# Optimization experiments

Measured on AMD Instinct MI355X. Metric: run time of the kernel, lower is better.

The kernel has to match this reference:

```python
import math
import jax, jax.numpy as jnp
import numpy as np

D = 1152      # vision_dim
P = 14        # patch
IMG = 896     # image_size
CIN = 3       # vision_channels
L = 2         # vision_blocks
MLP = 4304    # vision_mlp_hidden
EPS = 1e-6
B = 1
N = (IMG // P) ** 2  # 4096 tokens


def _ln(x, w, b):
    m = jnp.mean(x, axis=-1, keepdims=True)
    v = jnp.mean(jnp.square(x - m), axis=-1, keepdims=True)
    return (x - m) * jax.lax.rsqrt(v + EPS) * w + b


def setup_inputs() -> dict:
    key = jax.random.key(0)
    ks = jax.random.split(key, 20)
    s = 0.02
    inp = {
        "img": jax.random.normal(ks[0], (B, CIN, IMG, IMG), jnp.float32),
        "patch_w": jax.random.normal(ks[1], (D, CIN, P, P), jnp.float32) * s,
        "patch_b": jnp.zeros((D,), jnp.float32),
        "pos": jax.random.normal(ks[2], (D, N), jnp.float32) * s,
        # per-block params stacked along leading L axis (torch Linear: [out, in])
        "ln1_w": jnp.ones((L, D), jnp.float32),
        "ln1_b": jnp.zeros((L, D), jnp.float32),
        "qkv_w": jax.random.normal(ks[3], (L, 3 * D, D), jnp.float32) * s,
        "qkv_b": jnp.zeros((L, 3 * D), jnp.float32),
        "proj_w": jax.random.normal(ks[4], (L, D, D), jnp.float32) * s,
        "proj_b": jnp.zeros((L, D), jnp.float32),
        "ln2_w": jnp.ones((L, D), jnp.float32),
        "ln2_b": jnp.zeros((L, D), jnp.float32),
        "fc1_w": jax.random.normal(ks[5], (L, MLP, D), jnp.float32) * s,
        "fc1_b": jnp.zeros((L, MLP), jnp.float32),
        "fc2_w": jax.random.normal(ks[6], (L, D, MLP), jnp.float32) * s,
        "fc2_b": jnp.zeros((L, D), jnp.float32),
        "post_w": jnp.ones((D,), jnp.float32),
        "post_b": jnp.zeros((D,), jnp.float32),
    }
    return inp


def reference(img, patch_w, patch_b, pos, ln1_w, ln1_b, qkv_w, qkv_b,
              proj_w, proj_b, ln2_w, ln2_b, fc1_w, fc1_b, fc2_w, fc2_b,
              post_w, post_b):
    # conv patch embed (kernel=stride=P, valid padding)
    x = jax.lax.conv_general_dilated(
        img, patch_w, window_strides=(P, P), padding="VALID",
        dimension_numbers=("NCHW", "OIHW", "NCHW"))
    x = x + patch_b[None, :, None, None]
    x = x.reshape(B, D, N).transpose(0, 2, 1)          # [B, N, D]
    x = x + pos.T[None, :, :]

    scale = 1.0 / math.sqrt(D)

    def blk(x, p):
        l1w, l1b, qw, qb, pw, pb, l2w, l2b, f1w, f1b, f2w, f2b = p
        h = _ln(x, l1w, l1b)
        qkv = jnp.einsum("bnd,ed->bne", h, qw) + qb     # [B, N, 3D]
        q, k, v = jnp.split(qkv, 3, axis=-1)            # single-head, full D
        attn = jax.nn.softmax(jnp.einsum("bnd,bmd->bnm", q, k) * scale, axis=-1)
        y = jnp.einsum("bnm,bmd->bnd", attn, v)
        x = x + jnp.einsum("bnd,ed->bne", y, pw) + pb
        h = _ln(x, l2w, l2b)
        h = jax.nn.gelu(jnp.einsum("bnd,md->bnm", h, f1w) + f1b, approximate=False)
        x = x + jnp.einsum("bnm,dm->bnd", h, f2w) + f2b
        return x, None

    x, _ = jax.lax.scan(blk, x, (ln1_w, ln1_b, qkv_w, qkv_b, proj_w, proj_b,
                                 ln2_w, ln2_b, fc1_w, fc1_b, fc2_w, fc2_b))
    return _ln(x, post_w, post_b)
```

## Files before the change

### kernel.cpp

```cpp
#include <hip/hip_runtime.h>

#define NT 4096
#define DD 1152
#define D3 3456
#define MLP_R 4304
#define MLP_P 4352
#define KP 640

typedef unsigned short u16;
typedef short v8s __attribute__((ext_vector_type(8)));
typedef float v4f __attribute__((ext_vector_type(4)));

__device__ __forceinline__ u16 f2b(float f) {
    unsigned int u = __builtin_bit_cast(unsigned int, f);
    u += 0x7fffu + ((u >> 16) & 1u);
    return (u16)(u >> 16);
}
__device__ __forceinline__ float b2f(u16 s) {
    unsigned int u = ((unsigned int)s) << 16;
    return __builtin_bit_cast(float, u);
}

__device__ __forceinline__ void async16(const void* g, void* l) {
    __builtin_amdgcn_global_load_lds(
        (const __attribute__((address_space(1))) void*)g,
        (__attribute__((address_space(3))) void*)l, 16, 0, 0);
}

template<int EPI, int MT, int DBUF = 0>
__global__ __launch_bounds__(256)
void gemm_bt(const u16* __restrict__ A, int lda,
             const u16* __restrict__ B, int ldb, int Kdim,
             const float* __restrict__ bias, const float* __restrict__ aux,
             float* __restrict__ outf, u16* __restrict__ outb, int ldc,
             u16* __restrict__ vt, int NX)
{
    constexpr int JT = (MT == 128) ? 4 : 2;
    constexpr int AR = MT * 8 / 256;
    constexpr int NB = DBUF ? 2 : 1;

    __shared__ union SM {
        struct { u16 a[NB * MT * 64]; u16 b[NB * 128 * 64]; } st;
        float sc[4][64][17];
    } sm;

    const int b    = blockIdx.x;
    const int MY   = (gridDim.x >> 3) / NX;
    const int q    = b >> 3;
    const int m0   = ((b & 7) * MY + q % MY) * MT;
    const int n0   = (q / MY) * 128;

    const int tid  = threadIdx.x;
    const int lane = tid & 63;
    const int wave = tid >> 6;
    const int wm   = (MT == 128) ? (wave & 1) * 64 : 0;
    const int wn   = (MT == 128) ? (wave >> 1) * 64 : wave * 32;
    const int fr   = lane & 15;
    const int kqh  = lane >> 4;
    const int swz  = fr & 7;

    v4f acc[4][JT];
    const v4f vzero = {0.f, 0.f, 0.f, 0.f};
#pragma unroll
    for (int i = 0; i < 4; ++i)
#pragma unroll
        for (int j = 0; j < JT; ++j) acc[i][j] = vzero;

    auto stage = [&](u16* As, u16* Bs, int kt) {
#pragma unroll
        for (int r = 0; r < AR; ++r) {
            int c = r * 256 + tid;
            int row = c >> 3;
            int kc = (c & 7) ^ (row & 7);
            async16(A + (size_t)(m0 + row) * lda + kt + kc * 8, As + c * 8);
        }
#pragma unroll
        for (int r = 0; r < 4; ++r) {
            int c = r * 256 + tid;
            int row = c >> 3;
            int kc = (c & 7) ^ (row & 7);
            async16(B + (size_t)(n0 + row) * ldb + kt + kc * 8, Bs + c * 8);
        }
    };

    auto compute = [&](const u16* As, const u16* Bs) {
#pragma unroll
        for (int ks = 0; ks < 2; ++ks) {
            const int kq = ks * 4 + kqh;
            const int kp = (kq ^ swz) * 8;
            v8s af[4], bf[JT];
#pragma unroll
            for (int i = 0; i < 4; ++i)
                af[i] = *(const v8s*)(As + (wm + i * 16 + fr) * 64 + kp);
#pragma unroll
            for (int j = 0; j < JT; ++j)
                bf[j] = *(const v8s*)(Bs + (wn + j * 16 + fr) * 64 + kp);
#pragma unroll
            for (int i = 0; i < 4; ++i)
#pragma unroll
                for (int j = 0; j < JT; ++j)
                    acc[i][j] = __builtin_amdgcn_mfma_f32_16x16x32_bf16(
                        af[i], bf[j], acc[i][j], 0, 0, 0);
        }
    };

    if constexpr (DBUF) {
        stage(sm.st.a, sm.st.b, 0);
        int cur = 0;
        for (int kt = 0; kt < Kdim; kt += 64) {
            __syncthreads();
            const int nxt = cur ^ 1;
            if (kt + 64 < Kdim)
                stage(sm.st.a + nxt * (MT * 64), sm.st.b + nxt * (128 * 64), kt + 64);
            compute(sm.st.a + cur * (MT * 64), sm.st.b + cur * (128 * 64));
            cur = nxt;
        }
    } else {
        for (int kt = 0; kt < Kdim; kt += 64) {
            stage(sm.st.a, sm.st.b, kt);
            __syncthreads();
            compute(sm.st.a, sm.st.b);
            __syncthreads();
        }
    }

    const int cn = lane & 15;
    const int cm = (lane >> 4) * 4;
    float (*S)[17] = sm.sc[wave];
    const int gm = m0 + wm + lane;
#pragma unroll
    for (int jp = 0; jp < JT; ++jp) {
        __syncthreads();
#pragma unroll
        for (int i = 0; i < 4; ++i)
#pragma unroll
            for (int r = 0; r < 4; ++r)
                S[i * 16 + cm + r][cn] = acc[i][jp][r];
        __syncthreads();
        const int gn0 = n0 + wn + jp * 16;
        float v[16];
#pragma unroll
        for (int c = 0; c < 16; ++c) v[c] = S[lane][c];
        if constexpr (EPI <= 2) {
            union { u16 us[16]; uint4 q4[2]; } o;
#pragma unroll
            for (int c = 0; c < 16; ++c) {
                float t = v[c];
                if constexpr (EPI >= 1) t += bias[gn0 + c];
                if constexpr (EPI == 2) {
                    float u = t * (0.7978845608028654f + 0.03567740814183026f * t * t);
                    t = t / (1.0f + __expf(-2.0f * u));
                }
                o.us[c] = f2b(t);
            }
            uint4* dst = (uint4*)(outb + (size_t)gm * ldc + gn0);
            dst[0] = o.q4[0];
            dst[1] = o.q4[1];
            if constexpr (EPI == 1) {
                if (vt != nullptr && gn0 >= 2304) {
#pragma unroll
                    for (int c = 0; c < 16; ++c)
                        vt[(size_t)(gn0 + c - 2304) * NT + gm] = o.us[c];
                }
            }
        } else if constexpr (EPI == 3) {
            float* dst = outf + (size_t)gm * ldc + gn0;
            const float* ax = aux + (size_t)gm * ldc + gn0;
#pragma unroll
            for (int c = 0; c < 4; ++c) {
                float4 a4 = ((const float4*)ax)[c];
                float4 r4;
                r4.x = a4.x + v[4 * c + 0] + bias[gn0 + 4 * c + 0];
                r4.y = a4.y + v[4 * c + 1] + bias[gn0 + 4 * c + 1];
                r4.z = a4.z + v[4 * c + 2] + bias[gn0 + 4 * c + 2];
                r4.w = a4.w + v[4 * c + 3] + bias[gn0 + 4 * c + 3];
                ((float4*)dst)[c] = r4;
            }
        } else {
            float* dst = outf + (size_t)gm * ldc + gn0;
#pragma unroll
            for (int c = 0; c < 4; ++c) {
                float4 r4;
                r4.x = v[4 * c + 0] + bias[gn0 + 4 * c + 0] + aux[(size_t)(gn0 + 4 * c + 0) * NT + gm];
                r4.y = v[4 * c + 1] + bias[gn0 + 4 * c + 1] + aux[(size_t)(gn0 + 4 * c + 1) * NT + gm];
                r4.z = v[4 * c + 2] + bias[gn0 + 4 * c + 2] + aux[(size_t)(gn0 + 4 * c + 2) * NT + gm];
                r4.w = v[4 * c + 3] + bias[gn0 + 4 * c + 3] + aux[(size_t)(gn0 + 4 * c + 3) * NT + gm];
                ((float4*)dst)[c] = r4;
            }
        }
    }
}

template<int OUTF>
__global__ __launch_bounds__(384)
void ln_kernel(const float* __restrict__ x, const float* __restrict__ w,
               const float* __restrict__ b, void* __restrict__ out)
{
    const int n = blockIdx.x;
    const int t = threadIdx.x;
    const float* row = x + (size_t)n * DD;
    float v0 = row[t], v1 = row[t + 384], v2 = row[t + 768];
    float s  = v0 + v1 + v2;
    float ss = v0 * v0 + v1 * v1 + v2 * v2;
#pragma unroll
    for (int o = 32; o > 0; o >>= 1) {
        s  += __shfl_down(s, o);
        ss += __shfl_down(ss, o);
    }
    __shared__ float ps[6], pss[6], mh[2];
    if ((t & 63) == 0) { ps[t >> 6] = s; pss[t >> 6] = ss; }
    __syncthreads();
    if (t == 0) {
        float S = 0.f, SS = 0.f;
        for (int i = 0; i < 6; ++i) { S += ps[i]; SS += pss[i]; }
        float m = S / (float)DD;
        float var = SS / (float)DD - m * m;
        mh[0] = m;
        mh[1] = rsqrtf(var + 1e-6f);
    }
    __syncthreads();
    const float m = mh[0], rs = mh[1];
#pragma unroll
    for (int j = 0; j < 3; ++j) {
        int c = t + j * 384;
        float y = (row[c] - m) * rs * w[c] + b[c];
        if constexpr (OUTF) ((float*)out)[(size_t)n * DD + c] = y;
        else                ((u16*)out)[(size_t)n * DD + c]   = f2b(y);
    }
}

__global__ __launch_bounds__(256)
void softmax_kernel(u16* __restrict__ s)
{
    const float SC = 0.029462782549439484f;
    const int row = blockIdx.x;
    const int t = threadIdx.x;
    u16* p = s + (size_t)row * NT + t * 16;
    uint4 u0 = *(const uint4*)p;
    uint4 u1 = *(const uint4*)(p + 8);
    float v[16];
    unsigned int w[8] = {u0.x, u0.y, u0.z, u0.w, u1.x, u1.y, u1.z, u1.w};
#pragma unroll
    for (int i = 0; i < 8; ++i) {
        v[2 * i]     = b2f((u16)(w[i] & 0xffffu)) * SC;
        v[2 * i + 1] = b2f((u16)(w[i] >> 16)) * SC;
    }
    float mx = -1e30f;
#pragma unroll
    for (int i = 0; i < 16; ++i) mx = fmaxf(mx, v[i]);
#pragma unroll
    for (int o = 32; o > 0; o >>= 1) mx = fmaxf(mx, __shfl_down(mx, o));
    __shared__ float red[4];
    __shared__ float bc;
    if ((t & 63) == 0) red[t >> 6] = mx;
    __syncthreads();
    if (t == 0) bc = fmaxf(fmaxf(red[0], red[1]), fmaxf(red[2], red[3]));
    __syncthreads();
    const float M = bc;
    float sum = 0.f;
#pragma unroll
    for (int i = 0; i < 16; ++i) { v[i] = __expf(v[i] - M); sum += v[i]; }
#pragma unroll
    for (int o = 32; o > 0; o >>= 1) sum += __shfl_down(sum, o);
    __syncthreads();
    if ((t & 63) == 0) red[t >> 6] = sum;
    __syncthreads();
    if (t == 0) bc = red[0] + red[1] + red[2] + red[3];
    __syncthreads();
    const float inv = 1.0f / bc;
    union { u16 us[8]; uint4 u4; } o0, o1;
#pragma unroll
    for (int i = 0; i < 8; ++i) o0.us[i] = f2b(v[i] * inv);
#pragma unroll
    for (int i = 0; i < 8; ++i) o1.us[i] = f2b(v[8 + i] * inv);
    *(uint4*)p = o0.u4;
    *(uint4*)(p + 8) = o1.u4;
}

__global__ __launch_bounds__(256)
void im2col_kernel(const float* __restrict__ img, u16* __restrict__ a)
{
    const int k = blockIdx.x * 256 + threadIdx.x;
    const int n = blockIdx.y;
    if (k >= KP) return;
    float v = 0.f;
    if (k < 588) {
        int cin = k / 196;
        int rr = k - cin * 196;
        int py = rr / 14;
        int px = rr - py * 14;
        int gy = (n >> 6) * 14 + py;
        int gx = (n & 63) * 14 + px;
        v = img[(size_t)cin * 896 * 896 + (size_t)gy * 896 + gx];
    }
    a[(size_t)n * KP + k] = f2b(v);
}

constexpr int CV_S0 = 2 * D3 * DD / 4;
constexpr int CV_S1 = CV_S0 + 2 * DD * DD / 4;
constexpr int CV_S2 = CV_S1 + 2 * MLP_P * DD / 4;
constexpr int CV_S3 = CV_S2 + 2 * DD * MLP_P / 4;
constexpr int CV_S4 = CV_S3 + DD * KP / 4;
constexpr int CV_S5 = CV_S4 + 2 * MLP_P / 4;
constexpr int CV_BLOCKS = (CV_S5 + 255) / 256;

__device__ __forceinline__ void store_bf4(u16* p, float4 f) {
    union { u16 s[4]; uint2 d; } o;
    o.s[0] = f2b(f.x); o.s[1] = f2b(f.y); o.s[2] = f2b(f.z); o.s[3] = f2b(f.w);
    *(uint2*)p = o.d;
}

__global__ __launch_bounds__(256)
void convert_all(const float* __restrict__ qkv_w, const float* __restrict__ proj_w,
                 const float* __restrict__ fc1_w, const float* __restrict__ fc2_w,
                 const float* __restrict__ patch_w, const float* __restrict__ fc1_b,
                 u16* __restrict__ w_qkv, u16* __restrict__ w_proj,
                 u16* __restrict__ w_fc1, u16* __restrict__ w_fc2,
                 u16* __restrict__ w_pat, float* __restrict__ fc1b_p)
{
    int v = blockIdx.x * 256 + threadIdx.x;
    if (v >= CV_S5) return;
    const float4 z4 = {0.f, 0.f, 0.f, 0.f};
    if (v < CV_S0) {
        store_bf4(w_qkv + (size_t)v * 4, ((const float4*)qkv_w)[v]);
    } else if (v < CV_S1) {
        int e = v - CV_S0;
        store_bf4(w_proj + (size_t)e * 4, ((const float4*)proj_w)[e]);
    } else if (v < CV_S2) {
        size_t e = (size_t)(v - CV_S1) * 4;
        int row = (int)(e / DD);
        int c = (int)(e % DD);
        int l = row / MLP_P, lr = row % MLP_P;
        float4 f = z4;
        if (lr < MLP_R)
            f = *(const float4*)(fc1_w + ((size_t)l * MLP_R + lr) * DD + c);
        store_bf4(w_fc1 + e, f);
    } else if (v < CV_S3) {
        size_t e = (size_t)(v - CV_S2) * 4;
        int row = (int)(e / MLP_P);
        int c = (int)(e % MLP_P);
        float4 f = z4;
        if (c < MLP_R)
            f = *(const float4*)(fc2_w + (size_t)row * MLP_R + c);
        store_bf4(w_fc2 + e, f);
    } else if (v < CV_S4) {
        size_t e = (size_t)(v - CV_S3) * 4;
        int row = (int)(e / KP);
        int c = (int)(e % KP);
        float4 f = z4;
        if (c < 588)
            f = *(const float4*)(patch_w + (size_t)row * 588 + c);
        store_bf4(w_pat + e, f);
    } else {
        size_t e = (size_t)(v - CV_S4) * 4;
        int l = (int)(e / MLP_P);
        int c = (int)(e % MLP_P);
        float4 f = z4;
        if (c < MLP_R)
            f = *(const float4*)(fc1_b + (size_t)l * MLP_R + c);
        *(float4*)(fc1b_p + e) = f;
    }
}

constexpr size_t OFF_X      = 0;
constexpr size_t OFF_HBF    = OFF_X      + (size_t)NT * DD * 4;
constexpr size_t OFF_TMP    = OFF_HBF    + (size_t)NT * DD * 2;
constexpr size_t OFF_QKV    = OFF_TMP    + (size_t)NT * MLP_P * 2;
constexpr size_t OFF_VT     = OFF_QKV    + (size_t)NT * D3 * 2;
constexpr size_t OFF_IM     = OFF_VT     + (size_t)DD * NT * 2;
constexpr size_t OFF_WQKV   = OFF_IM     + (size_t)NT * KP * 2;
constexpr size_t OFF_WPROJ  = OFF_WQKV   + (size_t)2 * D3 * DD * 2;
constexpr size_t OFF_WFC1   = OFF_WPROJ  + (size_t)2 * DD * DD * 2;
constexpr size_t OFF_WFC2   = OFF_WFC1   + (size_t)2 * MLP_P * DD * 2;
constexpr size_t OFF_WPATCH = OFF_WFC2   + (size_t)2 * DD * MLP_P * 2;
constexpr size_t OFF_FC1B   = OFF_WPATCH + (size_t)DD * KP * 2;

extern "C" void kernel_launch(void* const* d_in, const int* in_sizes, int n_in,
                              void* d_out, int out_size, void* d_ws, size_t ws_size,
                              hipStream_t stream)
{
    const float* img     = (const float*)d_in[0];
    const float* patch_w = (const float*)d_in[1];
    const float* patch_b = (const float*)d_in[2];
    const float* pos     = (const float*)d_in[3];
    const float* ln1_w   = (const float*)d_in[4];
    const float* ln1_b   = (const float*)d_in[5];
    const float* qkv_w   = (const float*)d_in[6];
    const float* qkv_b   = (const float*)d_in[7];
    const float* proj_w  = (const float*)d_in[8];
    const float* proj_b  = (const float*)d_in[9];
    const float* ln2_w   = (const float*)d_in[10];
    const float* ln2_b   = (const float*)d_in[11];
    const float* fc1_w   = (const float*)d_in[12];
    const float* fc1_b   = (const float*)d_in[13];
    const float* fc2_w   = (const float*)d_in[14];
    const float* fc2_b   = (const float*)d_in[15];
    const float* post_w  = (const float*)d_in[16];
    const float* post_b  = (const float*)d_in[17];

    char* ws = (char*)d_ws;
    float* x      = (float*)(ws + OFF_X);
    u16*  h_bf    = (u16*)(ws + OFF_HBF);
    u16*  tmp_bf  = (u16*)(ws + OFF_TMP);
    u16*  qkv_bf  = (u16*)(ws + OFF_QKV);
    u16*  vt      = (u16*)(ws + OFF_VT);
    u16*  a_im    = (u16*)(ws + OFF_IM);
    u16*  w_qkv   = (u16*)(ws + OFF_WQKV);
    u16*  w_proj  = (u16*)(ws + OFF_WPROJ);
    u16*  w_fc1   = (u16*)(ws + OFF_WFC1);
    u16*  w_fc2   = (u16*)(ws + OFF_WFC2);
    u16*  w_pat   = (u16*)(ws + OFF_WPATCH);
    float* fc1b_p = (float*)(ws + OFF_FC1B);

    convert_all<<<CV_BLOCKS, 256, 0, stream>>>(
        qkv_w, proj_w, fc1_w, fc2_w, patch_w, fc1_b,
        w_qkv, w_proj, w_fc1, w_fc2, w_pat, fc1b_p);
    im2col_kernel<<<dim3(3, NT), 256, 0, stream>>>(img, a_im);

    gemm_bt<4, 64, 1><<<9 * 64, 256, 0, stream>>>(
        a_im, KP, w_pat, KP, KP, patch_b, pos, x, nullptr, DD, nullptr, 9);

    for (int l = 0; l < 2; ++l) {
        ln_kernel<0><<<NT, 384, 0, stream>>>(x, ln1_w + l * DD, ln1_b + l * DD, h_bf);
        gemm_bt<1, 128><<<27 * 32, 256, 0, stream>>>(
            h_bf, DD, w_qkv + (size_t)l * D3 * DD, DD, DD,
            qkv_b + (size_t)l * D3, nullptr, nullptr, qkv_bf, D3, vt, 27);
        gemm_bt<0, 128><<<32 * 32, 256, 0, stream>>>(
            qkv_bf, D3, qkv_bf + DD, D3, DD,
            nullptr, nullptr, nullptr, tmp_bf, NT, nullptr, 32);
        softmax_kernel<<<NT, 256, 0, stream>>>(tmp_bf);
        gemm_bt<0, 64, 1><<<9 * 64, 256, 0, stream>>>(
            tmp_bf, NT, vt, NT, NT, nullptr, nullptr, nullptr, h_bf, DD, nullptr, 9);
        gemm_bt<3, 64, 1><<<9 * 64, 256, 0, stream>>>(
            h_bf, DD, w_proj + (size_t)l * DD * DD, DD, DD,
            proj_b + (size_t)l * DD, x, x, nullptr, DD, nullptr, 9);
        ln_kernel<0><<<NT, 384, 0, stream>>>(x, ln2_w + l * DD, ln2_b + l * DD, h_bf);
        gemm_bt<2, 128><<<34 * 32, 256, 0, stream>>>(
            h_bf, DD, w_fc1 + (size_t)l * MLP_P * DD, DD, DD,
            fc1b_p + (size_t)l * MLP_P, nullptr, nullptr, tmp_bf, MLP_P, nullptr, 34);
        gemm_bt<3, 64, 1><<<9 * 64, 256, 0, stream>>>(
            tmp_bf, MLP_P, w_fc2 + (size_t)l * DD * MLP_P, MLP_P, MLP_P,
            fc2_b + (size_t)l * DD, x, x, nullptr, DD, nullptr, 9);
    }
    ln_kernel<1><<<NT, 384, 0, stream>>>(x, post_w, post_b, d_out);
}
```

Before: 919.5 us.

## Add 256x256 eight-wave pipelined GEMM for QK^T and FC1

Introduces a new 512-thread GEMM kernel with 256x256 output tiles, double-buffered async global-to-LDS loads, swizzled LDS layout, staged fragment loads interleaved with MFMA phases, priority bumps and a grid remap across XCDs. It replaces the 128-tile GEMM for the attention score product and the FC1+GELU layer. The larger tiles raise data reuse per loaded byte and overlap loads with compute, at the cost of fewer workgroups (256/272) and heavy register use that may limit occupancy.

```diff
diff --git a/kernel.cpp b/kernel.cpp
--- a/kernel.cpp
+++ b/kernel.cpp
@@ -25,6 +25,188 @@
     __builtin_amdgcn_global_load_lds(
         (const __attribute__((address_space(1))) void*)g,
         (__attribute__((address_space(3))) void*)l, 16, 0, 0);
+}
+
+__device__ __forceinline__ float gelu_f(float t) {
+    float u = t * (0.7978845608028654f + 0.03567740814183026f * t * t);
+    return t / (1.0f + __expf(-2.0f * u));
+}
+
+template<int EPI>
+__global__ __launch_bounds__(512, 2)
+void gemm8p(const u16* __restrict__ A, const u16* __restrict__ B, int ld,
+            int Kdim, const float* __restrict__ bias,
+            u16* __restrict__ outb, int ldc, int NNT)
+{
+    __shared__ __align__(128) union { u16 kl[2][32768]; u16 ep[8][8192]; } sm;
+    const int tid  = threadIdx.x, lane = tid & 63, wave = tid >> 6;
+    const int wr   = wave >> 2, wc = wave & 3;
+    const int fr   = lane & 15, kqh = lane >> 4;
+
+    const int nwg  = gridDim.x;
+    const int bidx = (int)blockIdx.x;
+    const int wg   = (bidx & 7) * (nwg >> 3) + (bidx >> 3);
+    const int mt   = wg / NNT, nt = wg % NNT;
+    const int bm0  = mt * 256, bn0 = nt * 256;
+
+    const int c    = tid;
+    const int s_lr = (c >> 7) * 16 + ((c >> 2) & 15);
+    const int s_lc = ((((c >> 6) & 1) * 4) + ((c & 3) ^ (((c >> 5) & 1) << 1))) * 8;
+    const size_t s_off = (size_t)s_lr * ld + s_lc;
+    const int koff = fr * 32 + ((kqh * 8) ^ ((fr & 8) << 1));
+
+    u16* kb = sm.kl[0];
+
+    auto stage = [&](int bi, int reg, const u16* gRowBase) {
+        u16* lb = kb + bi * 32768 + reg * 8192;
+        async16(gRowBase + s_off, lb + tid * 8);
+        async16(gRowBase + s_off + (size_t)64 * ld, lb + (512 + tid) * 8);
+    };
+    auto srcA = [&](int h, int t) { return A + (size_t)(bm0 + h * 128) * ld + t * 64; };
+    auto srcB = [&](int h, int t) { return B + (size_t)(bn0 + h * 128) * ld + t * 64; };
+
+    v4f acc[8][4];
+    const v4f vzero = {0.f, 0.f, 0.f, 0.f};
+#pragma unroll
+    for (int i = 0; i < 8; ++i)
+#pragma unroll
+        for (int j = 0; j < 4; ++j) acc[i][j] = vzero;
+
+    const int NKT = Kdim >> 6;
+
+    stage(0, 2, srcB(0, 0));
+    stage(0, 3, srcB(1, 0));
+    stage(0, 0, srcA(0, 0));
+    stage(0, 1, srcA(1, 0));
+    if (NKT > 1) {
+        stage(1, 2, srcB(0, 1));
+        stage(1, 3, srcB(1, 1));
+        asm volatile("s_waitcnt vmcnt(4)" ::: "memory");
+    } else {
+        asm volatile("s_waitcnt vmcnt(0)" ::: "memory");
+    }
+    asm volatile("s_barrier" ::: "memory");
+
+    v8s a[8], b0f[4], b1f[4];
+    for (int t = 0; t < NKT; ++t) {
+        const int bi = t & 1;
+        const int AR = bi * 32768 + wr * 8192;
+        const int BR = bi * 32768 + 16384 + (wc >> 1) * 8192;
+        const int bsub = (wc & 1) * 4;
+
+#pragma unroll
+        for (int mi = 0; mi < 4; ++mi)
+#pragma unroll
+            for (int ks = 0; ks < 2; ++ks)
+                a[mi * 2 + ks] = *(const v8s*)(kb + AR + (mi * 2 + ks) * 512 + koff);
+#pragma unroll
+        for (int nj = 0; nj < 2; ++nj)
+#pragma unroll
+            for (int ks = 0; ks < 2; ++ks)
+                b0f[nj * 2 + ks] = *(const v8s*)(kb + BR + ((bsub + nj) * 2 + ks) * 512 + koff);
+        if (t + 1 < NKT) stage(bi ^ 1, 0, srcA(0, t + 1));
+        asm volatile("s_barrier" ::: "memory");
+        asm volatile("s_waitcnt lgkmcnt(0)" ::: "memory");
+        __builtin_amdgcn_s_setprio(1);
+#pragma unroll
+        for (int mi = 0; mi < 4; ++mi)
+#pragma unroll
+            for (int nj = 0; nj < 2; ++nj)
+#pragma unroll
+                for (int ks = 0; ks < 2; ++ks)
+                    acc[mi][nj] = __builtin_amdgcn_mfma_f32_16x16x32_bf16(
+                        a[mi * 2 + ks], b0f[nj * 2 + ks], acc[mi][nj], 0, 0, 0);
+        __builtin_amdgcn_s_setprio(0);
+        asm volatile("s_barrier" ::: "memory");
+
+#pragma unroll
+        for (int nj = 0; nj < 2; ++nj)
+#pragma unroll
+            for (int ks = 0; ks < 2; ++ks)
+                b1f[nj * 2 + ks] = *(const v8s*)(kb + BR + ((bsub + 2 + nj) * 2 + ks) * 512 + koff);
+        if (t + 1 < NKT) stage(bi ^ 1, 1, srcA(1, t + 1));
+        asm volatile("s_barrier" ::: "memory");
+        asm volatile("s_waitcnt lgkmcnt(0)" ::: "memory");
+        __builtin_amdgcn_s_setprio(1);
+#pragma unroll
+        for (int mi = 0; mi < 4; ++mi)
+#pragma unroll
+            for (int nj = 0; nj < 2; ++nj)
+#pragma unroll
+                for (int ks = 0; ks < 2; ++ks)
+                    acc[mi][2 + nj] = __builtin_amdgcn_mfma_f32_16x16x32_bf16(
+                        a[mi * 2 + ks], b1f[nj * 2 + ks], acc[mi][2 + nj], 0, 0, 0);
+        __builtin_amdgcn_s_setprio(0);
+        asm volatile("s_barrier" ::: "memory");
+
+#pragma unroll
+        for (int mi = 0; mi < 4; ++mi)
+#pragma unroll
+            for (int ks = 0; ks < 2; ++ks)
+                a[mi * 2 + ks] = *(const v8s*)(kb + AR + ((4 + mi) * 2 + ks) * 512 + koff);
+        if (t + 2 < NKT) stage(bi, 2, srcB(0, t + 2));
+        asm volatile("s_barrier" ::: "memory");
+        asm volatile("s_waitcnt lgkmcnt(0)" ::: "memory");
+        __builtin_amdgcn_s_setprio(1);
+#pragma unroll
+        for (int mi = 0; mi < 4; ++mi)
+#pragma unroll
+            for (int nj = 0; nj < 2; ++nj)
+#pragma unroll
+                for (int ks = 0; ks < 2; ++ks)
+                    acc[4 + mi][2 + nj] = __builtin_amdgcn_mfma_f32_16x16x32_bf16(
+                        a[mi * 2 + ks], b1f[nj * 2 + ks], acc[4 + mi][2 + nj], 0, 0, 0);
+        __builtin_amdgcn_s_setprio(0);
+        asm volatile("s_barrier" ::: "memory");
+
+        if (t + 2 < NKT) stage(bi, 3, srcB(1, t + 2));
+        asm volatile("s_barrier" ::: "memory");
+        __builtin_amdgcn_s_setprio(1);
+#pragma unroll
+        for (int mi = 0; mi < 4; ++mi)
+#pragma unroll
+            for (int nj = 0; nj < 2; ++nj)
+#pragma unroll
+                for (int ks = 0; ks < 2; ++ks)
+                    acc[4 + mi][nj] = __builtin_amdgcn_mfma_f32_16x16x32_bf16(
+                        a[mi * 2 + ks], b0f[nj * 2 + ks], acc[4 + mi][nj], 0, 0, 0);
+        __builtin_amdgcn_s_setprio(0);
+        asm volatile("s_waitcnt vmcnt(4)" ::: "memory");
+        asm volatile("s_barrier" ::: "memory");
+    }
+
+    asm volatile("s_waitcnt vmcnt(0)" ::: "memory");
+    asm volatile("s_barrier" ::: "memory");
+    u16* ew = sm.ep[wave];
+    float bcol[4];
+    if constexpr (EPI >= 1) {
+#pragma unroll
+        for (int nj = 0; nj < 4; ++nj)
+            bcol[nj] = bias[bn0 + wc * 64 + nj * 16 + fr];
+    }
+#pragma unroll
+    for (int mi = 0; mi < 8; ++mi)
+#pragma unroll
+        for (int nj = 0; nj < 4; ++nj)
+#pragma unroll
+            for (int r = 0; r < 4; ++r) {
+                int row = mi * 16 + kqh * 4 + r;
+                int ec  = nj * 16 + fr;
+                float t = acc[mi][nj][r];
+                if constexpr (EPI >= 1) t += bcol[nj];
+                if constexpr (EPI == 2) t = gelu_f(t);
+                ew[row * 64 + (ec ^ (((row >> 2) & 3) << 4))] = f2b(t);
+            }
+    asm volatile("s_waitcnt lgkmcnt(0)" ::: "memory");
+#pragma unroll
+    for (int p = 0; p < 16; ++p) {
+        int row = p * 8 + (lane >> 3);
+        int key = (row >> 2) & 3;
+        v8s ch = *(const v8s*)(ew + row * 64 + (((lane & 7) * 8) ^ (key << 4)));
+        size_t gm = (size_t)(bm0 + wr * 128 + row);
+        int gc = bn0 + wc * 64 + (lane & 7) * 8;
+        *(uint4*)(outb + gm * ldc + gc) = __builtin_bit_cast(uint4, ch);
+    }
 }
 
 template<int EPI, int MT, int DBUF = 0>
@@ -147,10 +329,7 @@
             for (int c = 0; c < 16; ++c) {
                 float t = v[c];
                 if constexpr (EPI >= 1) t += bias[gn0 + c];
-                if constexpr (EPI == 2) {
-                    float u = t * (0.7978845608028654f + 0.03567740814183026f * t * t);
-                    t = t / (1.0f + __expf(-2.0f * u));
-                }
+                if constexpr (EPI == 2) t = gelu_f(t);
                 o.us[c] = f2b(t);
             }
             uint4* dst = (uint4*)(outb + (size_t)gm * ldc + gn0);
@@ -425,9 +604,8 @@
         gemm_bt<1, 128><<<27 * 32, 256, 0, stream>>>(
             h_bf, DD, w_qkv + (size_t)l * D3 * DD, DD, DD,
             qkv_b + (size_t)l * D3, nullptr, nullptr, qkv_bf, D3, vt, 27);
-        gemm_bt<0, 128><<<32 * 32, 256, 0, stream>>>(
-            qkv_bf, D3, qkv_bf + DD, D3, DD,
-            nullptr, nullptr, nullptr, tmp_bf, NT, nullptr, 32);
+        gemm8p<0><<<256, 512, 0, stream>>>(
+            qkv_bf, qkv_bf + DD, D3, DD, nullptr, tmp_bf, NT, 16);
         softmax_kernel<<<NT, 256, 0, stream>>>(tmp_bf);
         gemm_bt<0, 64, 1><<<9 * 64, 256, 0, stream>>>(
             tmp_bf, NT, vt, NT, NT, nullptr, nullptr, nullptr, h_bf, DD, nullptr, 9);
@@ -435,9 +613,9 @@
             h_bf, DD, w_proj + (size_t)l * DD * DD, DD, DD,
             proj_b + (size_t)l * DD, x, x, nullptr, DD, nullptr, 9);
         ln_kernel<0><<<NT, 384, 0, stream>>>(x, ln2_w + l * DD, ln2_b + l * DD, h_bf);
-        gemm_bt<2, 128><<<34 * 32, 256, 0, stream>>>(
-            h_bf, DD, w_fc1 + (size_t)l * MLP_P * DD, DD, DD,
-            fc1b_p + (size_t)l * MLP_P, nullptr, nullptr, tmp_bf, MLP_P, nullptr, 34);
+        gemm8p<2><<<272, 512, 0, stream>>>(
+            h_bf, w_fc1 + (size_t)l * MLP_P * DD, DD, DD,
+            fc1b_p + (size_t)l * MLP_P, tmp_bf, MLP_P, 17);
         gemm_bt<3, 64, 1><<<9 * 64, 256, 0, stream>>>(
             tmp_bf, MLP_P, w_fc2 + (size_t)l * DD * MLP_P, MLP_P, MLP_P,
             fc2_b + (size_t)l * DD, x, x, nullptr, DD, nullptr, 9);
```

Result: no change. 926.2 us (+0.7%).
